# Kernel tuning notes

Measured on AMD Instinct MI355X. Metric: run time of the kernel, lower is better.

The kernel has to match this reference:

```python
import jax, jax.numpy as jnp
import numpy as np

NUM_CATES = 3000
HIDDEN = 64
N_GROUPS = 4
N_LAYERS = 2
HOP_NUM = 4
ALPHA = 0.15
EPS = 1e-5
B, L = 256, 50


def setup_inputs() -> dict:
    key = jax.random.key(0)
    ks = jax.random.split(key, 12)
    cate_list = jax.random.randint(ks[0], (B, L), 0, NUM_CATES)
    # sparse-ish binary adjacency with self loops (avg degree ~30)
    adj = (jax.random.uniform(ks[1], (NUM_CATES, NUM_CATES)) < 0.01).astype(jnp.float32)
    adj = jnp.maximum(adj, jnp.eye(NUM_CATES, dtype=jnp.float32))
    kaiming = (2.0 / HIDDEN) ** 0.5
    emb = jax.random.normal(ks[2], (NUM_CATES, HIDDEN)) * kaiming   # embedding_cates.weight
    Wq = jax.random.normal(ks[3], (N_LAYERS, HIDDEN, HIDDEN)) * HIDDEN ** -0.5
    Wk = jax.random.normal(ks[4], (N_LAYERS, HIDDEN, HIDDEN)) * HIDDEN ** -0.5
    Wv = jax.random.normal(ks[5], (N_LAYERS, HIDDEN, HIDDEN)) * HIDDEN ** -0.5
    Wg = jax.random.normal(ks[6], (HIDDEN, N_GROUPS)) * kaiming     # group_func
    bg = jnp.zeros((N_GROUPS,), jnp.float32)
    Wp = jax.random.normal(ks[7], (NUM_CATES, 1)) * (2.0 / NUM_CATES) ** 0.5  # group_pool_func
    bp = jnp.zeros((1,), jnp.float32)
    gamma = jnp.ones((HIDDEN,), jnp.float32)                        # custom BatchNorm scale
    beta = jnp.zeros((HIDDEN,), jnp.float32)                        # custom BatchNorm shift
    return {"cate_list": cate_list, "adj": adj, "emb": emb, "Wq": Wq, "Wk": Wk,
            "Wv": Wv, "Wg": Wg, "bg": bg, "Wp": Wp, "bp": bp, "gamma": gamma, "beta": beta}


def _magna_layer(h, adj, Wq, Wk, Wv):
    # graph attention diffusion (MAGNA): masked attention + hop_num PPR-style diffusion
    q = h @ Wq
    k = h @ Wk
    v = h @ Wv
    scores = (q @ k.T) / jnp.sqrt(jnp.float32(HIDDEN))          # [N, N]
    scores = jnp.where(adj > 0, scores, jnp.float32(-1e9))
    A = jax.nn.softmax(scores, axis=-1)
    z = v
    for _ in range(HOP_NUM):
        z = (1.0 - ALPHA) * (A @ z) + ALPHA * v
    return h + z                                                 # residual


def reference(cate_list, adj, emb, Wq, Wk, Wv, Wg, bg, Wp, bp, gamma, beta):
    h = emb
    for l in range(N_LAYERS):
        h = _magna_layer(h, adj, Wq[l], Wk[l], Wv[l])
    graph = h                                                    # [N, H]
    score_cluster = jax.nn.softmax(graph @ Wg + bg, axis=1)      # [N, G]
    # sub_graph[g, n, h] = score[n, g] * graph[n, h]
    sub_graph = score_cluster.T[:, :, None] * graph[None]        # [G, N, H]
    # per-user gather (vectorized index_select over batch)
    seq_emb = jnp.moveaxis(sub_graph[:, cate_list, :], 1, 0)     # [B, G, L, H]
    mask = (cate_list == 0)[:, None, :, None]                    # [B, 1, L, 1]
    seq_emb = jnp.where(mask, jnp.float32(0.0), seq_emb)
    # custom BatchNorm: normalize sub_graph with per-user stats from seq_emb
    mean = seq_emb.mean(axis=(1, 2), keepdims=True)              # [B, 1, 1, H]
    var = seq_emb.var(axis=(1, 2), keepdims=True)
    user_sub_graph = (sub_graph[None] - mean) / jnp.sqrt(var + EPS) * gamma + beta  # [B, G, N, H]
    user_sub_graph = jnp.swapaxes(user_sub_graph, 3, 2)          # [B, G, H, N]
    out = user_sub_graph @ Wp + bp                               # [B, G, H, 1]  (dropout = identity, eval)
    return out[..., 0]                                           # squeeze -> [B, G, H]
```

## Files before the change

### kernel.cpp

```cpp
#include <hip/hip_runtime.h>

#define NC 3000
#define NP 3072
#define CAP 64
#define HD 64
#define NG 4
#define LQ 50
#define NB 256
#define NQ4 750
#define SBST (NG * HD + 1)
#define NBLK 768
#define NREP 96

__device__ __forceinline__ void stg(float* p, float v) {
  __hip_atomic_store(p, v, __ATOMIC_RELAXED, __HIP_MEMORY_SCOPE_AGENT);
}
__device__ __forceinline__ void stf(unsigned* p, unsigned v) {
  __hip_atomic_store(p, v, __ATOMIC_RELAXED, __HIP_MEMORY_SCOPE_AGENT);
}
__device__ __forceinline__ unsigned ldf(const unsigned* p) {
  return __hip_atomic_load(p, __ATOMIC_RELAXED, __HIP_MEMORY_SCOPE_AGENT);
}

__device__ __forceinline__ void gridbar(unsigned* __restrict__ slot,
                                        unsigned* __restrict__ rep, unsigned phase) {
  __syncthreads();
  const int tid = threadIdx.x;
  const int blk = blockIdx.x;
  if (blk == 0) {
    if (tid == 0) stf(&slot[0], phase);
    bool d0 = false, d1 = false, d2 = false;
    for (;;) {
      if (!d0) d0 = (ldf(&slot[tid]) >= phase);
      if (!d1) d1 = (ldf(&slot[tid + 256]) >= phase);
      if (!d2) d2 = (ldf(&slot[tid + 512]) >= phase);
      if (__syncthreads_and(d0 && d1 && d2)) break;
      __builtin_amdgcn_s_sleep(1);
    }
    if (tid < NREP) stf(&rep[tid * 16], phase);
  } else {
    if (tid == 0) {
      stf(&slot[blk], phase);
      while (ldf(&rep[(blk % NREP) * 16]) < phase) __builtin_amdgcn_s_sleep(1);
    }
    __syncthreads();
  }
  asm volatile("" ::: "memory");
}

#define GATHER8(acc, vreg, creg, zin, d)                                   \
  {                                                                        \
    int dro = ((d) + 7) & ~7;                                              \
    for (int e = 0; e < dro; e += 8) {                                     \
      float v0 = __shfl(vreg, e + 0), v1 = __shfl(vreg, e + 1);            \
      float v2 = __shfl(vreg, e + 2), v3 = __shfl(vreg, e + 3);            \
      float v4 = __shfl(vreg, e + 4), v5 = __shfl(vreg, e + 5);            \
      float v6 = __shfl(vreg, e + 6), v7 = __shfl(vreg, e + 7);            \
      int c0 = __shfl(creg, e + 0), c1 = __shfl(creg, e + 1);              \
      int c2 = __shfl(creg, e + 2), c3 = __shfl(creg, e + 3);              \
      int c4 = __shfl(creg, e + 4), c5 = __shfl(creg, e + 5);              \
      int c6 = __shfl(creg, e + 6), c7 = __shfl(creg, e + 7);              \
      float z0 = zin[c0 * HD + lane], z1 = zin[c1 * HD + lane];            \
      float z2 = zin[c2 * HD + lane], z3 = zin[c3 * HD + lane];            \
      float z4 = zin[c4 * HD + lane], z5 = zin[c5 * HD + lane];            \
      float z6 = zin[c6 * HD + lane], z7 = zin[c7 * HD + lane];            \
      acc += v0 * z0 + v1 * z1 + v2 * z2 + v3 * z3;                        \
      acc += v4 * z4 + v5 * z5 + v6 * z6 + v7 * z7;                        \
    }                                                                      \
  }

__device__ __forceinline__ float hopz(const float* __restrict__ zin, float vreg, int creg,
                                      int d, int lane, float vown) {
  float acc = 0.f;
  GATHER8(acc, vreg, creg, zin, d);
  return 0.85f * acc + 0.15f * vown;
}

__device__ __forceinline__ void qkv3(float h, const float* __restrict__ Wq,
                                     const float* __restrict__ Wk, const float* __restrict__ Wv,
                                     int lane, float& aq, float& ak, float& av) {
  aq = 0.f; ak = 0.f; av = 0.f;
#pragma unroll 16
  for (int f = 0; f < HD; ++f) {
    float hv = __shfl(h, f);
    aq += hv * Wq[f * HD + lane];
    ak += hv * Wk[f * HD + lane];
    av += hv * Wv[f * HD + lane];
  }
}

__device__ __forceinline__ float score_hop(const float* __restrict__ kbuf,
                                           const float* __restrict__ vsrc, float qreg, int creg,
                                           int d, int lane, float vown,
                                           float* __restrict__ zout, int row) {
  float acc = 0.f;
  const float4* kr = reinterpret_cast<const float4*>(kbuf + creg * HD);
#pragma unroll
  for (int i = 0; i < 16; ++i) {
    float4 k4 = kr[i];
    acc += __shfl(qreg, 4 * i + 0) * k4.x;
    acc += __shfl(qreg, 4 * i + 1) * k4.y;
    acc += __shfl(qreg, 4 * i + 2) * k4.z;
    acc += __shfl(qreg, 4 * i + 3) * k4.w;
  }
  float e = (lane < d) ? __expf(acc * 0.125f) : 0.f;
  float s = e;
#pragma unroll
  for (int off = 1; off < 64; off <<= 1) s += __shfl_xor(s, off);
  float vreg = (s > 0.f) ? e / s : 0.f;
  float hacc = 0.f;
  GATHER8(hacc, vreg, creg, vsrc, d);
  stg(zout + row * HD + lane, 0.85f * hacc + 0.15f * vown);
  return vreg;
}

__global__ __launch_bounds__(1024) void k_init(unsigned* __restrict__ slot,
                                               unsigned* __restrict__ rep,
                                               float* __restrict__ Sbp) {
  const int t = threadIdx.x;
  if (t < NBLK) stf(&slot[t], 0u);
  for (int i = t; i < NREP * 16; i += 1024) stf(&rep[i], 0u);
  for (int i = t; i < 4 * SBST; i += 1024)
    __hip_atomic_store(&Sbp[i], 0.f, __ATOMIC_RELAXED, __HIP_MEMORY_SCOPE_AGENT);
}

__global__ __launch_bounds__(256, 3) void k_mega(
    const int* __restrict__ cate, const float* __restrict__ adj, const float* __restrict__ emb,
    const float* __restrict__ Wq, const float* __restrict__ Wk, const float* __restrict__ Wv,
    const float* __restrict__ Wg, const float* __restrict__ bg, const float* __restrict__ Wp,
    const float* __restrict__ bp, const float* __restrict__ gamma, const float* __restrict__ beta,
    float* __restrict__ out, float* __restrict__ kf, float* __restrict__ vf,
    float* __restrict__ kf2, float* __restrict__ vf2,
    float* __restrict__ z1, float* __restrict__ z2, float* __restrict__ z3,
    float* __restrict__ z5, float* __restrict__ z6, float* __restrict__ z7,
    float* __restrict__ hf, float* __restrict__ s2, float* __restrict__ Sbp,
    unsigned* __restrict__ slot, unsigned* __restrict__ rep) {
  const int tid = threadIdx.x, lane = tid & 63, wave = tid >> 6;
  const int blk = blockIdx.x;
  const int row = blk * 4 + wave;
  const bool inC = (row < NC);

  __shared__ int slds[4][CAP];
  __shared__ float Sl[NG * HD];
  __shared__ float Wl[4];
  __shared__ int cs[LQ];
  __shared__ float red[8][HD];

  slds[wave][lane] = 0;
  int d = 0;
  if (inC) {
    const float4* arow = reinterpret_cast<const float4*>(adj + (size_t)row * NC);
    const unsigned long long mlane = (1ull << lane) - 1ull;
    int base = 0;
#pragma unroll 3
    for (int g = 0; g < 12; ++g) {
      int idx = g * 64 + lane;
      float4 a4 = (idx < NQ4) ? arow[idx] : make_float4(0.f, 0.f, 0.f, 0.f);
      unsigned long long b0 = __ballot(a4.x != 0.f);
      unsigned long long b1 = __ballot(a4.y != 0.f);
      unsigned long long b2 = __ballot(a4.z != 0.f);
      unsigned long long b3 = __ballot(a4.w != 0.f);
      if (a4.x != 0.f) { int s = base + __popcll(b0 & mlane); if (s < CAP) slds[wave][s] = 4 * idx + 0; }
      base += __popcll(b0);
      if (a4.y != 0.f) { int s = base + __popcll(b1 & mlane); if (s < CAP) slds[wave][s] = 4 * idx + 1; }
      base += __popcll(b1);
      if (a4.z != 0.f) { int s = base + __popcll(b2 & mlane); if (s < CAP) slds[wave][s] = 4 * idx + 2; }
      base += __popcll(b2);
      if (a4.w != 0.f) { int s = base + __popcll(b3 & mlane); if (s < CAP) slds[wave][s] = 4 * idx + 3; }
      base += __popcll(b3);
    }
    d = (base < CAP) ? base : CAP;
  }
  __syncthreads();
  const int creg = slds[wave][lane];
  float qreg = 0.f, vown = 0.f;
  if (inC) {
    float hreg = emb[row * HD + lane];
    float aq, ak, av;
    qkv3(hreg, Wq, Wk, Wv, lane, aq, ak, av);
    stg(kf + row * HD + lane, ak);
    stg(vf + row * HD + lane, av);
    qreg = aq;
    vown = av;
  }
  gridbar(slot, rep, 1);

  float vreg = 0.f;
  if (inC) vreg = score_hop(kf, vf, qreg, creg, d, lane, vown, z1, row);
  gridbar(slot, rep, 2);
  if (inC) stg(z2 + row * HD + lane, hopz(z1, vreg, creg, d, lane, vown));
  gridbar(slot, rep, 3);
  if (inC) stg(z3 + row * HD + lane, hopz(z2, vreg, creg, d, lane, vown));
  gridbar(slot, rep, 4);
  float h1 = 0.f;
  if (inC) {
    float z = hopz(z3, vreg, creg, d, lane, vown);
    h1 = emb[row * HD + lane] + z;
    float aq, ak, av;
    qkv3(h1, Wq + HD * HD, Wk + HD * HD, Wv + HD * HD, lane, aq, ak, av);
    stg(kf2 + row * HD + lane, ak);
    stg(vf2 + row * HD + lane, av);
    qreg = aq; vown = av;
  }
  gridbar(slot, rep, 5);
  if (inC) vreg = score_hop(kf2, vf2, qreg, creg, d, lane, vown, z5, row);
  gridbar(slot, rep, 6);
  if (inC) stg(z6 + row * HD + lane, hopz(z5, vreg, creg, d, lane, vown));
  gridbar(slot, rep, 7);
  if (inC) stg(z7 + row * HD + lane, hopz(z6, vreg, creg, d, lane, vown));
  gridbar(slot, rep, 8);
  if (tid < NG * HD) Sl[tid] = 0.f;
  if (tid < 4) Wl[tid] = 0.f;
  __syncthreads();
  if (inC) {
    float z = hopz(z7, vreg, creg, d, lane, vown);
    float h = h1 + z;
    stg(hf + row * HD + lane, h);
    float4 wg = *reinterpret_cast<const float4*>(Wg + lane * NG);
    float a0 = h * wg.x, a1 = h * wg.y, a2 = h * wg.z, a3 = h * wg.w;
#pragma unroll
    for (int off = 1; off < 64; off <<= 1) {
      a0 += __shfl_xor(a0, off); a1 += __shfl_xor(a1, off);
      a2 += __shfl_xor(a2, off); a3 += __shfl_xor(a3, off);
    }
    float lg0 = a0 + bg[0], lg1 = a1 + bg[1], lg2 = a2 + bg[2], lg3 = a3 + bg[3];
    float mx = fmaxf(fmaxf(lg0, lg1), fmaxf(lg2, lg3));
    float e0 = __expf(lg0 - mx), e1 = __expf(lg1 - mx), e2 = __expf(lg2 - mx), e3 = __expf(lg3 - mx);
    float inv = 1.f / (e0 + e1 + e2 + e3);
    float p0 = e0 * inv, p1 = e1 * inv, p2 = e2 * inv, p3 = e3 * inv;
    if (lane == 0) stg(s2 + row, p0 * p0 + p1 * p1 + p2 * p2 + p3 * p3);
    float w = Wp[row];
    atomicAdd(&Sl[0 * HD + lane], p0 * w * h);
    atomicAdd(&Sl[1 * HD + lane], p1 * w * h);
    atomicAdd(&Sl[2 * HD + lane], p2 * w * h);
    atomicAdd(&Sl[3 * HD + lane], p3 * w * h);
    if (lane == 0) Wl[wave] = w;
  }
  __syncthreads();
  if (blk * 4 < NC) {
    float* Sc = Sbp + (blk & 3) * SBST;
    if (tid < NG * HD) atomicAdd(&Sc[tid], Sl[tid]);
    if (tid == 0) atomicAdd(&Sc[NG * HD], Wl[0] + Wl[1] + Wl[2] + Wl[3]);
  }
  gridbar(slot, rep, 9);
  if (blk < NB) {
    if (tid < LQ) cs[tid] = cate[blk * LQ + tid];
    __syncthreads();
    float msum = 0.f, qsum = 0.f;
#pragma unroll 4
    for (int l = wave; l < LQ; l += 4) {
      int c = cs[l];
      if (c != 0) {
        float gv = hf[c * HD + lane];
        msum += gv;
        qsum += s2[c] * gv * gv;
      }
    }
    red[wave][lane] = msum;
    red[4 + wave][lane] = qsum;
    __syncthreads();
    if (wave == 0) {
      msum = red[0][lane] + red[1][lane] + red[2][lane] + red[3][lane];
      qsum = red[4][lane] + red[5][lane] + red[6][lane] + red[7][lane];
      const float cntf = 1.f / (NG * LQ);
      float mean = msum * cntf;
      float var = fmaxf(qsum * cntf - mean * mean, 0.f);
      float invs = rsqrtf(var + 1e-5f);
      float gam = gamma[lane], bet = beta[lane], bpv = bp[0];
      float wsum = Sbp[NG * HD] + Sbp[SBST + NG * HD] + Sbp[2 * SBST + NG * HD] + Sbp[3 * SBST + NG * HD];
#pragma unroll
      for (int g = 0; g < NG; ++g) {
        float sg = Sbp[0 * SBST + g * HD + lane] + Sbp[1 * SBST + g * HD + lane] +
                   Sbp[2 * SBST + g * HD + lane] + Sbp[3 * SBST + g * HD + lane];
        out[blk * (NG * HD) + g * HD + lane] = invs * gam * (sg - mean * wsum) + bet * wsum + bpv;
      }
    }
  }
}

extern "C" void kernel_launch(void* const* d_in, const int* in_sizes, int n_in,
                              void* d_out, int out_size, void* d_ws, size_t ws_size,
                              hipStream_t stream) {
  const int* cate = (const int*)d_in[0];
  const float* adj = (const float*)d_in[1];
  const float* emb = (const float*)d_in[2];
  const float* Wq = (const float*)d_in[3];
  const float* Wk = (const float*)d_in[4];
  const float* Wv = (const float*)d_in[5];
  const float* Wg = (const float*)d_in[6];
  const float* bg = (const float*)d_in[7];
  const float* Wp = (const float*)d_in[8];
  const float* bp = (const float*)d_in[9];
  const float* gamma = (const float*)d_in[10];
  const float* beta = (const float*)d_in[11];
  float* out = (float*)d_out;

  char* p = (char*)d_ws;
  auto carve = [&](size_t bytes) { char* r = p; p += (bytes + 255) & ~(size_t)255; return r; };
  float* kf = (float*)carve((size_t)NP * HD * 4);
  float* vf = (float*)carve((size_t)NP * HD * 4);
  float* kf2 = (float*)carve((size_t)NP * HD * 4);
  float* vf2 = (float*)carve((size_t)NP * HD * 4);
  float* z1 = (float*)carve((size_t)NP * HD * 4);
  float* z2 = (float*)carve((size_t)NP * HD * 4);
  float* z3 = (float*)carve((size_t)NP * HD * 4);
  float* z5 = (float*)carve((size_t)NP * HD * 4);
  float* z6 = (float*)carve((size_t)NP * HD * 4);
  float* z7 = (float*)carve((size_t)NP * HD * 4);
  float* hf = (float*)carve((size_t)NP * HD * 4);
  float* s2 = (float*)carve((size_t)NP * 4);
  float* Sbp = (float*)carve((size_t)4 * SBST * 4);
  unsigned* slot = (unsigned*)carve((size_t)NBLK * 4);
  unsigned* rep = (unsigned*)carve((size_t)NREP * 16 * 4);

  k_init<<<1, 1024, 0, stream>>>(slot, rep, Sbp);
  k_mega<<<NBLK, 256, 0, stream>>>(cate, adj, emb, Wq, Wk, Wv, Wg, bg, Wp, bp, gamma, beta,
                                   out, kf, vf, kf2, vf2, z1, z2, z3, z5, z6, z7,
                                   hf, s2, Sbp, slot, rep);
}
```

Baseline: 173.2 us.

## Use 256 blocks of 12 waves and store attention weights in LDS

The persistent kernel now launches 256 blocks of 768 threads (12 rows each) instead of 768 blocks of 256 threads. That cuts the number of participants in each of the nine grid barriers and lets one thread per block-0 slot poll. The per-row column indices and softmax weights now live in LDS as int2 pairs, so the diffusion hops read them directly instead of broadcasting them with cross-lane shuffles. The partial-sum buffers rise from 4 to 8 to spread atomic contention. The trade-off is one block per CU with larger blocks, which depends on all 256 blocks being co-resident, plus more LDS use.

```diff
diff --git a/kernel.cpp b/kernel.cpp
--- a/kernel.cpp
+++ b/kernel.cpp
@@ -9,8 +9,11 @@
 #define NB 256
 #define NQ4 750
 #define SBST (NG * HD + 1)
-#define NBLK 768
-#define NREP 96
+#define NSBC 8
+#define NBLK 256
+#define TPB 768
+#define WPB 12
+#define NREP 32
 
 __device__ __forceinline__ void stg(float* p, float v) {
   __hip_atomic_store(p, v, __ATOMIC_RELAXED, __HIP_MEMORY_SCOPE_AGENT);
@@ -29,50 +32,39 @@
   const int blk = blockIdx.x;
   if (blk == 0) {
     if (tid == 0) stf(&slot[0], phase);
-    bool d0 = false, d1 = false, d2 = false;
+    bool dn = (tid >= NBLK);
     for (;;) {
-      if (!d0) d0 = (ldf(&slot[tid]) >= phase);
-      if (!d1) d1 = (ldf(&slot[tid + 256]) >= phase);
-      if (!d2) d2 = (ldf(&slot[tid + 512]) >= phase);
-      if (__syncthreads_and(d0 && d1 && d2)) break;
+      if (!dn) dn = (ldf(&slot[tid]) >= phase);
+      if (__syncthreads_and(dn)) break;
       __builtin_amdgcn_s_sleep(1);
     }
     if (tid < NREP) stf(&rep[tid * 16], phase);
   } else {
     if (tid == 0) {
       stf(&slot[blk], phase);
-      while (ldf(&rep[(blk % NREP) * 16]) < phase) __builtin_amdgcn_s_sleep(1);
+      while (ldf(&rep[(blk & (NREP - 1)) * 16]) < phase) __builtin_amdgcn_s_sleep(1);
     }
     __syncthreads();
   }
   asm volatile("" ::: "memory");
 }
 
-#define GATHER8(acc, vreg, creg, zin, d)                                   \
-  {                                                                        \
-    int dro = ((d) + 7) & ~7;                                              \
-    for (int e = 0; e < dro; e += 8) {                                     \
-      float v0 = __shfl(vreg, e + 0), v1 = __shfl(vreg, e + 1);            \
-      float v2 = __shfl(vreg, e + 2), v3 = __shfl(vreg, e + 3);            \
-      float v4 = __shfl(vreg, e + 4), v5 = __shfl(vreg, e + 5);            \
-      float v6 = __shfl(vreg, e + 6), v7 = __shfl(vreg, e + 7);            \
-      int c0 = __shfl(creg, e + 0), c1 = __shfl(creg, e + 1);              \
-      int c2 = __shfl(creg, e + 2), c3 = __shfl(creg, e + 3);              \
-      int c4 = __shfl(creg, e + 4), c5 = __shfl(creg, e + 5);              \
-      int c6 = __shfl(creg, e + 6), c7 = __shfl(creg, e + 7);              \
-      float z0 = zin[c0 * HD + lane], z1 = zin[c1 * HD + lane];            \
-      float z2 = zin[c2 * HD + lane], z3 = zin[c3 * HD + lane];            \
-      float z4 = zin[c4 * HD + lane], z5 = zin[c5 * HD + lane];            \
-      float z6 = zin[c6 * HD + lane], z7 = zin[c7 * HD + lane];            \
-      acc += v0 * z0 + v1 * z1 + v2 * z2 + v3 * z3;                        \
-      acc += v4 * z4 + v5 * z5 + v6 * z6 + v7 * z7;                        \
-    }                                                                      \
-  }
-
-__device__ __forceinline__ float hopz(const float* __restrict__ zin, float vreg, int creg,
+__device__ __forceinline__ float hopz(const float* __restrict__ zin, const int2* scvw,
                                       int d, int lane, float vown) {
   float acc = 0.f;
-  GATHER8(acc, vreg, creg, zin, d);
+  const int dro = (d + 7) & ~7;
+  for (int e = 0; e < dro; e += 8) {
+    int2 a0 = scvw[e + 0], a1 = scvw[e + 1], a2 = scvw[e + 2], a3 = scvw[e + 3];
+    int2 a4 = scvw[e + 4], a5 = scvw[e + 5], a6 = scvw[e + 6], a7 = scvw[e + 7];
+    float z0 = zin[a0.x * HD + lane], z1 = zin[a1.x * HD + lane];
+    float z2 = zin[a2.x * HD + lane], z3 = zin[a3.x * HD + lane];
+    float z4 = zin[a4.x * HD + lane], z5 = zin[a5.x * HD + lane];
+    float z6 = zin[a6.x * HD + lane], z7 = zin[a7.x * HD + lane];
+    acc += __int_as_float(a0.y) * z0 + __int_as_float(a1.y) * z1
+         + __int_as_float(a2.y) * z2 + __int_as_float(a3.y) * z3;
+    acc += __int_as_float(a4.y) * z4 + __int_as_float(a5.y) * z5
+         + __int_as_float(a6.y) * z6 + __int_as_float(a7.y) * z7;
+  }
   return 0.85f * acc + 0.15f * vown;
 }
 
@@ -89,10 +81,10 @@
   }
 }
 
-__device__ __forceinline__ float score_hop(const float* __restrict__ kbuf,
-                                           const float* __restrict__ vsrc, float qreg, int creg,
-                                           int d, int lane, float vown,
-                                           float* __restrict__ zout, int row) {
+__device__ __forceinline__ void score_hop(const float* __restrict__ kbuf,
+                                          const float* __restrict__ vsrc, float qreg, int creg,
+                                          int d, int lane, float vown,
+                                          float* __restrict__ zout, int row, int2* scvw) {
   float acc = 0.f;
   const float4* kr = reinterpret_cast<const float4*>(kbuf + creg * HD);
 #pragma unroll
@@ -108,10 +100,9 @@
 #pragma unroll
   for (int off = 1; off < 64; off <<= 1) s += __shfl_xor(s, off);
   float vreg = (s > 0.f) ? e / s : 0.f;
-  float hacc = 0.f;
-  GATHER8(hacc, vreg, creg, vsrc, d);
-  stg(zout + row * HD + lane, 0.85f * hacc + 0.15f * vown);
-  return vreg;
+  scvw[lane] = make_int2(creg, __float_as_int(vreg));
+  float hacc = hopz(vsrc, scvw, d, lane, vown);
+  stg(zout + row * HD + lane, hacc);
 }
 
 __global__ __launch_bounds__(1024) void k_init(unsigned* __restrict__ slot,
@@ -120,11 +111,11 @@
   const int t = threadIdx.x;
   if (t < NBLK) stf(&slot[t], 0u);
   for (int i = t; i < NREP * 16; i += 1024) stf(&rep[i], 0u);
-  for (int i = t; i < 4 * SBST; i += 1024)
+  for (int i = t; i < NSBC * SBST; i += 1024)
     __hip_atomic_store(&Sbp[i], 0.f, __ATOMIC_RELAXED, __HIP_MEMORY_SCOPE_AGENT);
 }
 
-__global__ __launch_bounds__(256, 3) void k_mega(
+__global__ __launch_bounds__(TPB, 1) void k_mega(
     const int* __restrict__ cate, const float* __restrict__ adj, const float* __restrict__ emb,
     const float* __restrict__ Wq, const float* __restrict__ Wk, const float* __restrict__ Wv,
     const float* __restrict__ Wg, const float* __restrict__ bg, const float* __restrict__ Wp,
@@ -137,16 +128,16 @@
     unsigned* __restrict__ slot, unsigned* __restrict__ rep) {
   const int tid = threadIdx.x, lane = tid & 63, wave = tid >> 6;
   const int blk = blockIdx.x;
-  const int row = blk * 4 + wave;
+  const int row = blk * WPB + wave;
   const bool inC = (row < NC);
 
-  __shared__ int slds[4][CAP];
+  __shared__ int2 scv[WPB][CAP];
   __shared__ float Sl[NG * HD];
-  __shared__ float Wl[4];
+  __shared__ float Wl[WPB];
   __shared__ int cs[LQ];
-  __shared__ float red[8][HD];
-
-  slds[wave][lane] = 0;
+  __shared__ float red[2 * WPB][HD];
+
+  scv[wave][lane] = make_int2(0, 0);
   int d = 0;
   if (inC) {
     const float4* arow = reinterpret_cast<const float4*>(adj + (size_t)row * NC);
@@ -160,19 +151,19 @@
       unsigned long long b1 = __ballot(a4.y != 0.f);
       unsigned long long b2 = __ballot(a4.z != 0.f);
       unsigned long long b3 = __ballot(a4.w != 0.f);
-      if (a4.x != 0.f) { int s = base + __popcll(b0 & mlane); if (s < CAP) slds[wave][s] = 4 * idx + 0; }
+      if (a4.x != 0.f) { int s = base + __popcll(b0 & mlane); if (s < CAP) scv[wave][s].x = 4 * idx + 0; }
       base += __popcll(b0);
-      if (a4.y != 0.f) { int s = base + __popcll(b1 & mlane); if (s < CAP) slds[wave][s] = 4 * idx + 1; }
+      if (a4.y != 0.f) { int s = base + __popcll(b1 & mlane); if (s < CAP) scv[wave][s].x = 4 * idx + 1; }
       base += __popcll(b1);
-      if (a4.z != 0.f) { int s = base + __popcll(b2 & mlane); if (s < CAP) slds[wave][s] = 4 * idx + 2; }
+      if (a4.z != 0.f) { int s = base + __popcll(b2 & mlane); if (s < CAP) scv[wave][s].x = 4 * idx + 2; }
       base += __popcll(b2);
-      if (a4.w != 0.f) { int s = base + __popcll(b3 & mlane); if (s < CAP) slds[wave][s] = 4 * idx + 3; }
+      if (a4.w != 0.f) { int s = base + __popcll(b3 & mlane); if (s < CAP) scv[wave][s].x = 4 * idx + 3; }
       base += __popcll(b3);
     }
     d = (base < CAP) ? base : CAP;
   }
-  __syncthreads();
-  const int creg = slds[wave][lane];
+  const int creg = scv[wave][lane].x;
+  int2* scvw = &scv[wave][0];
   float qreg = 0.f, vown = 0.f;
   if (inC) {
     float hreg = emb[row * HD + lane];
@@ -185,16 +176,15 @@
   }
   gridbar(slot, rep, 1);
 
-  float vreg = 0.f;
-  if (inC) vreg = score_hop(kf, vf, qreg, creg, d, lane, vown, z1, row);
+  if (inC) score_hop(kf, vf, qreg, creg, d, lane, vown, z1, row, scvw);
   gridbar(slot, rep, 2);
-  if (inC) stg(z2 + row * HD + lane, hopz(z1, vreg, creg, d, lane, vown));
+  if (inC) stg(z2 + row * HD + lane, hopz(z1, scvw, d, lane, vown));
   gridbar(slot, rep, 3);
-  if (inC) stg(z3 + row * HD + lane, hopz(z2, vreg, creg, d, lane, vown));
+  if (inC) stg(z3 + row * HD + lane, hopz(z2, scvw, d, lane, vown));
   gridbar(slot, rep, 4);
   float h1 = 0.f;
   if (inC) {
-    float z = hopz(z3, vreg, creg, d, lane, vown);
+    float z = hopz(z3, scvw, d, lane, vown);
     h1 = emb[row * HD + lane] + z;
     float aq, ak, av;
     qkv3(h1, Wq + HD * HD, Wk + HD * HD, Wv + HD * HD, lane, aq, ak, av);
@@ -203,17 +193,17 @@
     qreg = aq; vown = av;
   }
   gridbar(slot, rep, 5);
-  if (inC) vreg = score_hop(kf2, vf2, qreg, creg, d, lane, vown, z5, row);
+  if (inC) score_hop(kf2, vf2, qreg, creg, d, lane, vown, z5, row, scvw);
   gridbar(slot, rep, 6);
-  if (inC) stg(z6 + row * HD + lane, hopz(z5, vreg, creg, d, lane, vown));
+  if (inC) stg(z6 + row * HD + lane, hopz(z5, scvw, d, lane, vown));
   gridbar(slot, rep, 7);
-  if (inC) stg(z7 + row * HD + lane, hopz(z6, vreg, creg, d, lane, vown));
+  if (inC) stg(z7 + row * HD + lane, hopz(z6, scvw, d, lane, vown));
   gridbar(slot, rep, 8);
   if (tid < NG * HD) Sl[tid] = 0.f;
-  if (tid < 4) Wl[tid] = 0.f;
+  if (tid < WPB) Wl[tid] = 0.f;
   __syncthreads();
   if (inC) {
-    float z = hopz(z7, vreg, creg, d, lane, vown);
+    float z = hopz(z7, scvw, d, lane, vown);
     float h = h1 + z;
     stg(hf + row * HD + lane, h);
     float4 wg = *reinterpret_cast<const float4*>(Wg + lane * NG);
@@ -237,18 +227,22 @@
     if (lane == 0) Wl[wave] = w;
   }
   __syncthreads();
-  if (blk * 4 < NC) {
-    float* Sc = Sbp + (blk & 3) * SBST;
+  if (blk * WPB < NC) {
+    float* Sc = Sbp + (blk & (NSBC - 1)) * SBST;
     if (tid < NG * HD) atomicAdd(&Sc[tid], Sl[tid]);
-    if (tid == 0) atomicAdd(&Sc[NG * HD], Wl[0] + Wl[1] + Wl[2] + Wl[3]);
+    if (tid == 0) {
+      float ws = 0.f;
+#pragma unroll
+      for (int i = 0; i < WPB; ++i) ws += Wl[i];
+      atomicAdd(&Sc[NG * HD], ws);
+    }
   }
   gridbar(slot, rep, 9);
   if (blk < NB) {
     if (tid < LQ) cs[tid] = cate[blk * LQ + tid];
     __syncthreads();
     float msum = 0.f, qsum = 0.f;
-#pragma unroll 4
-    for (int l = wave; l < LQ; l += 4) {
+    for (int l = wave; l < LQ; l += WPB) {
       int c = cs[l];
       if (c != 0) {
         float gv = hf[c * HD + lane];
@@ -257,21 +251,25 @@
       }
     }
     red[wave][lane] = msum;
-    red[4 + wave][lane] = qsum;
+    red[WPB + wave][lane] = qsum;
     __syncthreads();
     if (wave == 0) {
-      msum = red[0][lane] + red[1][lane] + red[2][lane] + red[3][lane];
-      qsum = red[4][lane] + red[5][lane] + red[6][lane] + red[7][lane];
+      msum = 0.f; qsum = 0.f;
+#pragma unroll
+      for (int i = 0; i < WPB; ++i) { msum += red[i][lane]; qsum += red[WPB + i][lane]; }
       const float cntf = 1.f / (NG * LQ);
       float mean = msum * cntf;
       float var = fmaxf(qsum * cntf - mean * mean, 0.f);
       float invs = rsqrtf(var + 1e-5f);
       float gam = gamma[lane], bet = beta[lane], bpv = bp[0];
-      float wsum = Sbp[NG * HD] + Sbp[SBST + NG * HD] + Sbp[2 * SBST + NG * HD] + Sbp[3 * SBST + NG * HD];
+      float wsum = 0.f;
+#pragma unroll
+      for (int i = 0; i < NSBC; ++i) wsum += Sbp[i * SBST + NG * HD];
 #pragma unroll
       for (int g = 0; g < NG; ++g) {
-        float sg = Sbp[0 * SBST + g * HD + lane] + Sbp[1 * SBST + g * HD + lane] +
-                   Sbp[2 * SBST + g * HD + lane] + Sbp[3 * SBST + g * HD + lane];
+        float sg = 0.f;
+#pragma unroll
+        for (int i = 0; i < NSBC; ++i) sg += Sbp[i * SBST + g * HD + lane];
         out[blk * (NG * HD) + g * HD + lane] = invs * gam * (sg - mean * wsum) + bet * wsum + bpv;
       }
     }
@@ -309,12 +307,12 @@
   float* z7 = (float*)carve((size_t)NP * HD * 4);
   float* hf = (float*)carve((size_t)NP * HD * 4);
   float* s2 = (float*)carve((size_t)NP * 4);
-  float* Sbp = (float*)carve((size_t)4 * SBST * 4);
+  float* Sbp = (float*)carve((size_t)NSBC * SBST * 4);
   unsigned* slot = (unsigned*)carve((size_t)NBLK * 4);
   unsigned* rep = (unsigned*)carve((size_t)NREP * 16 * 4);
 
   k_init<<<1, 1024, 0, stream>>>(slot, rep, Sbp);
-  k_mega<<<NBLK, 256, 0, stream>>>(cate, adj, emb, Wq, Wk, Wv, Wg, bg, Wp, bp, gamma, beta,
+  k_mega<<<NBLK, TPB, 0, stream>>>(cate, adj, emb, Wq, Wk, Wv, Wg, bg, Wp, bp, gamma, beta,
                                    out, kf, vf, kf2, vf2, z1, z2, z3, z5, z6, z7,
                                    hf, s2, Sbp, slot, rep);
 }
```

Result: faster. 156.7 us (-9.5%).
